# Performance work log

Hardware: AMD Instinct MI355X
Metric: run time of the kernel (lower is better)

The kernel has to match this reference:

```python
import jax, jax.numpy as jnp
import numpy as np

N_P, N_W = 50000, 10000          # protein / pathway node counts
D_P, D_W = 256, 128              # input feature dims
HID, OUT, K, L = 64, 8, 4, 2     # hidden, out, heads, layers
E_PP, E_PW, E_WP = 500000, 150000, 150000


def setup_inputs() -> dict:
    ks = jax.random.split(jax.random.key(0), 16)
    s = 0.1

    def edges(k, e, n_src, n_dst):
        k1, k2 = jax.random.split(k)
        return jnp.stack([
            jax.random.randint(k1, (e,), 0, n_src, dtype=jnp.int32),
            jax.random.randint(k2, (e,), 0, n_dst, dtype=jnp.int32),
        ])

    return {
        "x_protein": jax.random.normal(ks[0], (N_P, D_P), jnp.float32),
        "x_pathway": jax.random.normal(ks[1], (N_W, D_W), jnp.float32),
        "W_proj_p": jax.random.normal(ks[2], (D_P, HID), jnp.float32) * s,
        "b_proj_p": jnp.zeros((HID,), jnp.float32),
        "W_proj_w": jax.random.normal(ks[3], (D_W, HID), jnp.float32) * s,
        "b_proj_w": jnp.zeros((HID,), jnp.float32),
        # per layer, per edge type (0: p->p, 1: p->w, 2: w->p)
        "W_src": jax.random.normal(ks[4], (L, 3, HID, K * HID), jnp.float32) * s,
        "W_dst": jax.random.normal(ks[5], (L, 3, HID, K * HID), jnp.float32) * s,
        "att_src": jax.random.normal(ks[6], (L, 3, K, HID), jnp.float32) * s,
        "att_dst": jax.random.normal(ks[7], (L, 3, K, HID), jnp.float32) * s,
        "conv_bias": jnp.zeros((L, 3, HID), jnp.float32),
        "W_post_p": jax.random.normal(ks[8], (HID, OUT), jnp.float32) * s,
        "b_post_p": jnp.zeros((OUT,), jnp.float32),
        "W_post_w": jax.random.normal(ks[9], (HID, OUT), jnp.float32) * s,
        "b_post_w": jnp.zeros((OUT,), jnp.float32),
        "ei_pp": edges(ks[10], E_PP, N_P, N_P),
        "ei_pw": edges(ks[11], E_PW, N_P, N_W),
        "ei_wp": edges(ks[12], E_WP, N_W, N_P),
    }


def _gat(h_src, h_dst, edge, Wsrc, Wdst, asrc, adst, bias, n_dst):
    """PyG GATConv((-1,-1), HID, heads=K, concat=False, add_self_loops=False)."""
    hs = (h_src @ Wsrc).reshape(-1, K, HID)           # [Ns, K, H]
    hd = (h_dst @ Wdst).reshape(-1, K, HID)           # [Nd, K, H]
    a_s = jnp.sum(hs * asrc, axis=-1)                 # [Ns, K]
    a_d = jnp.sum(hd * adst, axis=-1)                 # [Nd, K]
    src, dst = edge[0], edge[1]
    e = jax.nn.leaky_relu(a_s[src] + a_d[dst], 0.2)   # [E, K]
    # segment softmax over destination neighborhoods
    m = jax.ops.segment_max(e, dst, num_segments=n_dst)
    ex = jnp.exp(e - m[dst])
    denom = jax.ops.segment_sum(ex, dst, num_segments=n_dst)
    alpha = ex / denom[dst]                           # [E, K]
    msg = hs[src] * alpha[:, :, None]                 # [E, K, H]
    out = jax.ops.segment_sum(msg, dst, num_segments=n_dst)  # [Nd, K, H]
    return out.mean(axis=1) + bias                    # concat=False -> head mean


def reference(x_protein, x_pathway, W_proj_p, b_proj_p, W_proj_w, b_proj_w,
              W_src, W_dst, att_src, att_dst, conv_bias,
              W_post_p, b_post_p, W_post_w, b_post_w,
              ei_pp, ei_pw, ei_wp):
    # eval mode: all dropouts are identity
    h_p = x_protein @ W_proj_p + b_proj_p
    h_w = x_pathway @ W_proj_w + b_proj_w
    for l in range(L):
        o_pp = _gat(h_p, h_p, ei_pp, W_src[l, 0], W_dst[l, 0],
                    att_src[l, 0], att_dst[l, 0], conv_bias[l, 0], N_P)
        o_pw = _gat(h_p, h_w, ei_pw, W_src[l, 1], W_dst[l, 1],
                    att_src[l, 1], att_dst[l, 1], conv_bias[l, 1], N_W)
        o_wp = _gat(h_w, h_p, ei_wp, W_src[l, 2], W_dst[l, 2],
                    att_src[l, 2], att_dst[l, 2], conv_bias[l, 2], N_P)
        # HeteroConv aggr='mean': protein receives p->p and w->p; pathway receives p->w
        h_p = jax.nn.elu((o_pp + o_wp) * 0.5)
        h_w = jax.nn.elu(o_pw)
    out_p = h_p @ W_post_p + b_post_p
    out_w = h_w @ W_post_w + b_post_w
    return out_p, out_w
```

## Files before the change

kernel.cpp:

```cpp
#include <hip/hip_runtime.h>
#include <hip/hip_fp16.h>
#include <cfloat>
#include <cmath>

#define N_P 50000
#define N_W 10000
#define D_P 256
#define D_W 128
#define HID 64
#define OUTD 8
#define KH 4
#define LL 2
#define E_PP 500000
#define E_PW 150000
#define E_WP 150000
#define NTOT (N_P + N_W + N_P)
#define ETOT (E_PP + E_PW + E_WP)
#define NBP ((N_P + 63) / 64)
#define NBW ((N_W + 63) / 64)

typedef _Float16 f16x8 __attribute__((ext_vector_type(8)));
typedef float f32x4 __attribute__((ext_vector_type(4)));

__device__ inline float lrelu02(float v) { return v > 0.f ? v : 0.2f * v; }

__device__ inline f16x8 ld8h(const _Float16* p) { return *(const f16x8*)p; }
__device__ inline f16x8 ld8h(const __half* p) { return *(const f16x8*)p; }
__device__ inline f16x8 ld8h(const float* p) {
    float4 lo = *(const float4*)p;
    float4 hi = *(const float4*)(p + 4);
    f16x8 a = { (_Float16)lo.x, (_Float16)lo.y, (_Float16)lo.z, (_Float16)lo.w,
                (_Float16)hi.x, (_Float16)hi.y, (_Float16)hi.z, (_Float16)hi.w };
    return a;
}

template<typename AT, bool ELU>
__device__ inline void gemm64_core(const AT* __restrict__ A, const __half* __restrict__ Bt,
                                   const float* __restrict__ bias,
                                   float* __restrict__ C, __half* __restrict__ C16,
                                   int M, int K, int bid) {
    int lane = threadIdx.x & 63;
    int wv = threadIdx.x >> 6;
    int rbase = bid * 64 + wv * 16;
    int arow = min(rbase + (lane & 15), M - 1);
    int kgrp = (lane >> 4) * 8;
    const AT* Ap = A + (size_t)arow * K + kgrp;
    const _Float16* Bp = (const _Float16*)Bt + kgrp;
    int bcol = lane & 15;

    f32x4 acc0 = {0.f, 0.f, 0.f, 0.f};
    f32x4 acc1 = {0.f, 0.f, 0.f, 0.f};
    f32x4 acc2 = {0.f, 0.f, 0.f, 0.f};
    f32x4 acc3 = {0.f, 0.f, 0.f, 0.f};

#pragma unroll 4
    for (int k0 = 0; k0 < K; k0 += 32) {
        f16x8 a = ld8h(Ap + k0);
        f16x8 b0 = *(const f16x8*)(Bp + (size_t)(0 * 16 + bcol) * K + k0);
        f16x8 b1 = *(const f16x8*)(Bp + (size_t)(1 * 16 + bcol) * K + k0);
        f16x8 b2 = *(const f16x8*)(Bp + (size_t)(2 * 16 + bcol) * K + k0);
        f16x8 b3 = *(const f16x8*)(Bp + (size_t)(3 * 16 + bcol) * K + k0);
        acc0 = __builtin_amdgcn_mfma_f32_16x16x32_f16(a, b0, acc0, 0, 0, 0);
        acc1 = __builtin_amdgcn_mfma_f32_16x16x32_f16(a, b1, acc1, 0, 0, 0);
        acc2 = __builtin_amdgcn_mfma_f32_16x16x32_f16(a, b2, acc2, 0, 0, 0);
        acc3 = __builtin_amdgcn_mfma_f32_16x16x32_f16(a, b3, acc3, 0, 0, 0);
    }

    int crow = rbase + (lane >> 4) * 4;
    f32x4 accs[4] = {acc0, acc1, acc2, acc3};
#pragma unroll
    for (int t = 0; t < 4; ++t) {
        int col = t * 16 + (lane & 15);
        float bv = bias[col];
#pragma unroll
        for (int r = 0; r < 4; ++r) {
            int rr = crow + r;
            if (rr < M) {
                float v = accs[t][r] + bv;
                if (ELU) v = v > 0.f ? v : expf(v) - 1.f;
                C[(size_t)rr * 64 + col] = v;
                C16[(size_t)rr * 64 + col] = __float2half(v);
            }
        }
    }
}

__global__ __launch_bounds__(256) void mfma_proj2(
    const float* __restrict__ xp, const float* __restrict__ xw,
    const __half* __restrict__ wtP, const __half* __restrict__ wtW,
    const float* __restrict__ bpp, const float* __restrict__ bpw,
    float* __restrict__ hp, __half* __restrict__ hp16,
    float* __restrict__ hw, __half* __restrict__ hw16) {
    if (blockIdx.x < NBP)
        gemm64_core<float, false>(xp, wtP, bpp, hp, hp16, N_P, D_P, blockIdx.x);
    else
        gemm64_core<float, false>(xw, wtW, bpw, hw, hw16, N_W, D_W, blockIdx.x - NBP);
}

__global__ __launch_bounds__(256) void mfma_postagg2(
    const __half* __restrict__ aggp, const __half* __restrict__ aggw,
    const __half* __restrict__ wtp, const __half* __restrict__ wtw,
    const float* __restrict__ bp, const float* __restrict__ bw,
    float* __restrict__ hp, __half* __restrict__ hp16,
    float* __restrict__ hw, __half* __restrict__ hw16) {
    if (blockIdx.x < NBP)
        gemm64_core<__half, true>(aggp, wtp, bp, hp, hp16, N_P, 512, blockIdx.x);
    else
        gemm64_core<__half, true>(aggw, wtw, bw, hw, hw16, N_W, 256, blockIdx.x - NBP);
}

__device__ inline void agg_range(int base, int len, const int* __restrict__ perm,
                                 const float4* __restrict__ alpha,
                                 const __half* __restrict__ h16,
                                 int lane, int wv,
                                 float4 (*s_al)[64], int (*s_sr)[64],
                                 float& a0, float& a1, float& a2, float& a3) {
    for (int c0 = 0; c0 < len; c0 += 64) {
        int i = c0 + lane;
        if (i < len) {
            s_sr[wv][lane] = perm[base + i];
            s_al[wv][lane] = alpha[base + i];
        }
        int cnt = min(64, len - c0);
        int j = 0;
        for (; j + 4 <= cnt; j += 4) {
            int sj0 = s_sr[wv][j], sj1 = s_sr[wv][j + 1];
            int sj2 = s_sr[wv][j + 2], sj3 = s_sr[wv][j + 3];
            float h0 = __half2float(h16[(size_t)sj0 * HID + lane]);
            float h1 = __half2float(h16[(size_t)sj1 * HID + lane]);
            float h2 = __half2float(h16[(size_t)sj2 * HID + lane]);
            float h3 = __half2float(h16[(size_t)sj3 * HID + lane]);
            float4 l0 = s_al[wv][j], l1 = s_al[wv][j + 1];
            float4 l2 = s_al[wv][j + 2], l3 = s_al[wv][j + 3];
            a0 = fmaf(l0.x, h0, a0); a1 = fmaf(l0.y, h0, a1);
            a2 = fmaf(l0.z, h0, a2); a3 = fmaf(l0.w, h0, a3);
            a0 = fmaf(l1.x, h1, a0); a1 = fmaf(l1.y, h1, a1);
            a2 = fmaf(l1.z, h1, a2); a3 = fmaf(l1.w, h1, a3);
            a0 = fmaf(l2.x, h2, a0); a1 = fmaf(l2.y, h2, a1);
            a2 = fmaf(l2.z, h2, a2); a3 = fmaf(l2.w, h2, a3);
            a0 = fmaf(l3.x, h3, a0); a1 = fmaf(l3.y, h3, a1);
            a2 = fmaf(l3.z, h3, a2); a3 = fmaf(l3.w, h3, a3);
        }
        for (; j < cnt; ++j) {
            int sj = s_sr[wv][j];
            float4 al = s_al[wv][j];
            float hv = __half2float(h16[(size_t)sj * HID + lane]);
            a0 = fmaf(al.x, hv, a0); a1 = fmaf(al.y, hv, a1);
            a2 = fmaf(al.z, hv, a2); a3 = fmaf(al.w, hv, a3);
        }
    }
}

__global__ __launch_bounds__(256) void gat_msg_all(
    const int* __restrict__ rowptr, const int* __restrict__ perm,
    const float4* __restrict__ alpha, const float4* __restrict__ inv,
    const __half* __restrict__ hp16, const __half* __restrict__ hw16,
    __half* __restrict__ agg_p, __half* __restrict__ agg_w) {
    __shared__ float4 s_al[4][64];
    __shared__ int s_sr[4][64];
    int lane = threadIdx.x & 63;
    int wv = threadIdx.x >> 6;
    int d = (blockIdx.x << 2) + wv;
    if (d >= N_P + N_W) return;

    if (d < N_P) {
        float a0 = 0.f, a1 = 0.f, a2 = 0.f, a3 = 0.f;
        float b0 = 0.f, b1 = 0.f, b2 = 0.f, b3 = 0.f;
        int g1 = d, g2 = N_P + N_W + d;
        int base1 = rowptr[g1], len1 = rowptr[g1 + 1] - base1;
        int base2 = rowptr[g2], len2 = rowptr[g2 + 1] - base2;
        agg_range(base1, len1, perm, alpha, hp16, lane, wv, s_al, s_sr, a0, a1, a2, a3);
        agg_range(base2, len2, perm, alpha, hw16, lane, wv, s_al, s_sr, b0, b1, b2, b3);
        float4 i1 = inv[g1], i2 = inv[g2];
        size_t ob = (size_t)d * 512 + lane;
        agg_p[ob]       = __float2half(a0 * i1.x);
        agg_p[ob + 64]  = __float2half(a1 * i1.y);
        agg_p[ob + 128] = __float2half(a2 * i1.z);
        agg_p[ob + 192] = __float2half(a3 * i1.w);
        agg_p[ob + 256] = __float2half(b0 * i2.x);
        agg_p[ob + 320] = __float2half(b1 * i2.y);
        agg_p[ob + 384] = __float2half(b2 * i2.z);
        agg_p[ob + 448] = __float2half(b3 * i2.w);
    } else {
        int d2 = d - N_P;
        int g = N_P + d2;
        float a0 = 0.f, a1 = 0.f, a2 = 0.f, a3 = 0.f;
        int base = rowptr[g], len = rowptr[g + 1] - base;
        agg_range(base, len, perm, alpha, hp16, lane, wv, s_al, s_sr, a0, a1, a2, a3);
        float4 iv = inv[g];
        size_t ob = (size_t)d2 * 256 + lane;
        agg_w[ob]       = __float2half(a0 * iv.x);
        agg_w[ob + 64]  = __float2half(a1 * iv.y);
        agg_w[ob + 128] = __float2half(a2 * iv.z);
        agg_w[ob + 192] = __float2half(a3 * iv.w);
    }
}

template<int NJ>
__global__ void av_multi(const float* __restrict__ h,
                         const float* __restrict__ W0, const float* __restrict__ W1,
                         const float* __restrict__ W2, const float* __restrict__ W3,
                         float4* __restrict__ o0, float4* __restrict__ o1,
                         float4* __restrict__ o2, float4* __restrict__ o3, int M) {
    int n = blockIdx.x * blockDim.x + threadIdx.x;
    if (n >= M) return;
    const float4* h4 = (const float4*)(h + (size_t)n * HID);
    float a0[4] = {0.f, 0.f, 0.f, 0.f}, a1[4] = {0.f, 0.f, 0.f, 0.f};
    float a2[4] = {0.f, 0.f, 0.f, 0.f}, a3[4] = {0.f, 0.f, 0.f, 0.f};
#pragma unroll
    for (int k4 = 0; k4 < 16; ++k4) {
        float4 hv = h4[k4];
        float hvv[4] = {hv.x, hv.y, hv.z, hv.w};
#pragma unroll
        for (int r = 0; r < 4; ++r) {
            int f = k4 * 4 + r;
            float x = hvv[r];
#pragma unroll
            for (int c = 0; c < 4; ++c) a0[c] = fmaf(x, W0[f * 4 + c], a0[c]);
#pragma unroll
            for (int c = 0; c < 4; ++c) a1[c] = fmaf(x, W1[f * 4 + c], a1[c]);
            if (NJ > 2) {
#pragma unroll
                for (int c = 0; c < 4; ++c) a2[c] = fmaf(x, W2[f * 4 + c], a2[c]);
#pragma unroll
                for (int c = 0; c < 4; ++c) a3[c] = fmaf(x, W3[f * 4 + c], a3[c]);
            }
        }
    }
    o0[n] = make_float4(a0[0], a0[1], a0[2], a0[3]);
    o1[n] = make_float4(a1[0], a1[1], a1[2], a1[3]);
    if (NJ > 2) {
        o2[n] = make_float4(a2[0], a2[1], a2[2], a2[3]);
        o3[n] = make_float4(a3[0], a3[1], a3[2], a3[3]);
    }
}

__global__ void wv_kernel(const float* __restrict__ W, const float* __restrict__ att,
                          float* __restrict__ wv) {
    int lt = blockIdx.x;
    int j = threadIdx.x >> 2, k = threadIdx.x & 3;
    const float* Wp = W + (size_t)lt * HID * (KH * HID) + (size_t)j * (KH * HID) + k * HID;
    const float* ap = att + (size_t)lt * KH * HID + k * HID;
    float s = 0.f;
    for (int h = 0; h < HID; ++h) s += Wp[h] * ap[h];
    wv[(size_t)lt * HID * KH + j * KH + k] = s;
}

__global__ void build_wt_proj(const float* __restrict__ Wpp, const float* __restrict__ Wpw,
                              __half* __restrict__ wtP, __half* __restrict__ wtW) {
    int t = blockIdx.x * blockDim.x + threadIdx.x;
    if (t < 64 * 256) {
        int c = t >> 8, k = t & 255;
        wtP[t] = __float2half(Wpp[k * 64 + c]);
    } else if (t < 64 * 256 + 64 * 128) {
        int u = t - 64 * 256;
        int c = u >> 7, k = u & 127;
        wtW[u] = __float2half(Wpw[k * 64 + c]);
    }
}

__global__ void build_wcomb16(const float* __restrict__ Wsrc, const float* __restrict__ cbias,
                              __half* __restrict__ wtp, float* __restrict__ bp,
                              __half* __restrict__ wtw, float* __restrict__ bw) {
    int t = blockIdx.x * blockDim.x + threadIdx.x;
    const int P = LL * 64 * 512;
    if (t < P) {
        int l = t / (64 * 512);
        int rem = t % (64 * 512);
        int h = rem >> 9, r = rem & 511;
        int part = r >> 8, k = (r & 255) >> 6, j = r & 63;
        int type = (part == 0) ? 0 : 2;
        wtp[t] = __float2half(Wsrc[(((size_t)l * 3 + type) * 64 + j) * 256 + k * 64 + h] * 0.125f);
    } else if (t < P + LL * 64 * 256) {
        int u = t - P;
        int l = u / (64 * 256);
        int rem = u % (64 * 256);
        int h = rem >> 8, r = rem & 255;
        int k = r >> 6, j = r & 63;
        wtw[u] = __float2half(Wsrc[(((size_t)l * 3 + 1) * 64 + j) * 256 + k * 64 + h] * 0.25f);
    }
    if (t < LL * 64) {
        int l = t >> 6, c = t & 63;
        bp[t] = 0.5f * (cbias[(l * 3 + 0) * 64 + c] + cbias[(l * 3 + 2) * 64 + c]);
        bw[t] = cbias[(l * 3 + 1) * 64 + c];
    }
}

__global__ void count3_kernel(const int* __restrict__ ei_pp, const int* __restrict__ ei_pw,
                              const int* __restrict__ ei_wp, int* __restrict__ cnt) {
    int e = blockIdx.x * blockDim.x + threadIdx.x;
    if (e >= ETOT) return;
    const int* ei; int eo, no, E;
    if (e < E_PP) { ei = ei_pp; eo = 0; no = 0; E = E_PP; }
    else if (e < E_PP + E_PW) { ei = ei_pw; eo = E_PP; no = N_P; E = E_PW; }
    else { ei = ei_wp; eo = E_PP + E_PW; no = N_P + N_W; E = E_WP; }
    int el = e - eo;
    atomicAdd(&cnt[no + ei[E + el]], 1);
}

__global__ __launch_bounds__(1024) void block_sum_kernel(const int* __restrict__ cnt,
                                                         int* __restrict__ bsum, int n) {
    __shared__ int wsum[16];
    int tid = threadIdx.x, lane = tid & 63, wv = tid >> 6;
    int i = blockIdx.x * 1024 + tid;
    int v = (i < n) ? cnt[i] : 0;
#pragma unroll
    for (int off = 32; off > 0; off >>= 1) v += __shfl_xor(v, off, 64);
    if (lane == 0) wsum[wv] = v;
    __syncthreads();
    if (tid == 0) {
        int t = 0;
#pragma unroll
        for (int k = 0; k < 16; ++k) t += wsum[k];
        bsum[blockIdx.x] = t;
    }
}

__global__ __launch_bounds__(1024) void scan_bsums_kernel(int* __restrict__ bsum, int nb) {
    __shared__ int wsum[16], wexc[16];
    int tid = threadIdx.x, lane = tid & 63, wv = tid >> 6;
    int v = (tid < nb) ? bsum[tid] : 0;
    int x = v;
#pragma unroll
    for (int off = 1; off < 64; off <<= 1) {
        int y = __shfl_up(x, off, 64);
        if (lane >= off) x += y;
    }
    if (lane == 63) wsum[wv] = x;
    __syncthreads();
    if (wv == 0 && lane < 16) {
        int s = wsum[lane];
        int xx = s;
#pragma unroll
        for (int off = 1; off < 16; off <<= 1) {
            int y = __shfl_up(xx, off, 16);
            if (lane >= off) xx += y;
        }
        wexc[lane] = xx - s;
    }
    __syncthreads();
    if (tid < nb) bsum[tid] = x - v + wexc[wv];
}

__global__ __launch_bounds__(1024) void block_scan_kernel(const int* __restrict__ cnt,
                                                          const int* __restrict__ bsum,
                                                          int* __restrict__ rowptr,
                                                          int* __restrict__ woff, int n) {
    __shared__ int wsum[16], wexc[16];
    int tid = threadIdx.x, lane = tid & 63, wv = tid >> 6;
    int i = blockIdx.x * 1024 + tid;
    int v = (i < n) ? cnt[i] : 0;
    int x = v;
#pragma unroll
    for (int off = 1; off < 64; off <<= 1) {
        int y = __shfl_up(x, off, 64);
        if (lane >= off) x += y;
    }
    if (lane == 63) wsum[wv] = x;
    __syncthreads();
    if (wv == 0 && lane < 16) {
        int s = wsum[lane];
        int xx = s;
#pragma unroll
        for (int off = 1; off < 16; off <<= 1) {
            int y = __shfl_up(xx, off, 16);
            if (lane >= off) xx += y;
        }
        wexc[lane] = xx - s;
    }
    __syncthreads();
    int excl = x - v + wexc[wv] + bsum[blockIdx.x];
    if (i < n) { rowptr[i] = excl; woff[i] = excl; }
    if (i == n - 1) rowptr[n] = excl + v;
}

__global__ void scatter3_kernel(const int* __restrict__ ei_pp, const int* __restrict__ ei_pw,
                                const int* __restrict__ ei_wp, int* __restrict__ woff,
                                int* __restrict__ perm) {
    int e = blockIdx.x * blockDim.x + threadIdx.x;
    if (e >= ETOT) return;
    const int* ei; int eo, no, E;
    if (e < E_PP) { ei = ei_pp; eo = 0; no = 0; E = E_PP; }
    else if (e < E_PP + E_PW) { ei = ei_pw; eo = E_PP; no = N_P; E = E_PW; }
    else { ei = ei_wp; eo = E_PP + E_PW; no = N_P + N_W; E = E_WP; }
    int el = e - eo;
    int p = atomicAdd(&woff[no + ei[E + el]], 1);
    perm[p] = ei[el];
}

__global__ void gat_stats3(const int* __restrict__ rowptr, const int* __restrict__ perm,
                           const float4* __restrict__ a_pp_s, const float4* __restrict__ a_pp_d,
                           const float4* __restrict__ a_pw_s, const float4* __restrict__ a_pw_d,
                           const float4* __restrict__ a_wp_s, const float4* __restrict__ a_wp_d,
                           float4* __restrict__ alpha, float4* __restrict__ inv) {
    int g = blockIdx.x * blockDim.x + threadIdx.x;
    if (g >= NTOT) return;
    const float4 *as, *ad; int d;
    if (g < N_P) { as = a_pp_s; ad = a_pp_d; d = g; }
    else if (g < N_P + N_W) { as = a_pw_s; ad = a_pw_d; d = g - N_P; }
    else { as = a_wp_s; ad = a_wp_d; d = g - (N_P + N_W); }
    int base = rowptr[g], end = rowptr[g + 1];
    float4 adv = ad[d];
    float4 sm = make_float4(0.f, 0.f, 0.f, 0.f);
    for (int i = base; i < end; ++i) {
        float4 asv = as[perm[i]];
        float4 t;
        t.x = __expf(lrelu02(asv.x + adv.x));
        t.y = __expf(lrelu02(asv.y + adv.y));
        t.z = __expf(lrelu02(asv.z + adv.z));
        t.w = __expf(lrelu02(asv.w + adv.w));
        alpha[i] = t;
        sm.x += t.x; sm.y += t.y; sm.z += t.z; sm.w += t.w;
    }
    float4 iv;
    int len = end - base;
    iv.x = len ? 1.f / sm.x : 0.f;
    iv.y = len ? 1.f / sm.y : 0.f;
    iv.z = len ? 1.f / sm.z : 0.f;
    iv.w = len ? 1.f / sm.w : 0.f;
    inv[g] = iv;
}

__global__ void post_out(const float* __restrict__ h_p, const float* __restrict__ h_w,
                         const float* __restrict__ Wp, const float* __restrict__ bpv,
                         const float* __restrict__ Ww, const float* __restrict__ bwv,
                         float* __restrict__ out) {
    int n = blockIdx.x * blockDim.x + threadIdx.x;
    if (n >= N_P + N_W) return;
    const float *h, *W, *bb; float* o;
    if (n < N_P) { h = h_p + (size_t)n * HID; W = Wp; bb = bpv; o = out + (size_t)n * OUTD; }
    else { int m = n - N_P; h = h_w + (size_t)m * HID; W = Ww; bb = bwv; o = out + (size_t)N_P * OUTD + (size_t)m * OUTD; }
    const float4* h4 = (const float4*)h;
    float acc[OUTD];
#pragma unroll
    for (int c = 0; c < OUTD; ++c) acc[c] = bb[c];
#pragma unroll
    for (int k4 = 0; k4 < HID / 4; ++k4) {
        float4 hv = h4[k4];
#pragma unroll
        for (int c = 0; c < OUTD; ++c) {
            acc[c] = fmaf(hv.x, W[(k4 * 4 + 0) * OUTD + c], acc[c]);
            acc[c] = fmaf(hv.y, W[(k4 * 4 + 1) * OUTD + c], acc[c]);
            acc[c] = fmaf(hv.z, W[(k4 * 4 + 2) * OUTD + c], acc[c]);
            acc[c] = fmaf(hv.w, W[(k4 * 4 + 3) * OUTD + c], acc[c]);
        }
    }
#pragma unroll
    for (int c4 = 0; c4 < OUTD / 4; ++c4)
        *(float4*)&o[c4 * 4] = make_float4(acc[c4 * 4], acc[c4 * 4 + 1], acc[c4 * 4 + 2], acc[c4 * 4 + 3]);
}

extern "C" void kernel_launch(void* const* d_in, const int* in_sizes, int n_in,
                              void* d_out, int out_size, void* d_ws, size_t ws_size,
                              hipStream_t stream) {
    const float* x_p    = (const float*)d_in[0];
    const float* x_w    = (const float*)d_in[1];
    const float* Wpp    = (const float*)d_in[2];
    const float* bpp    = (const float*)d_in[3];
    const float* Wpw    = (const float*)d_in[4];
    const float* bpw    = (const float*)d_in[5];
    const float* Wsrc   = (const float*)d_in[6];
    const float* Wdst   = (const float*)d_in[7];
    const float* Asrc   = (const float*)d_in[8];
    const float* Adst   = (const float*)d_in[9];
    const float* cbias  = (const float*)d_in[10];
    const float* Wpostp = (const float*)d_in[11];
    const float* bpostp = (const float*)d_in[12];
    const float* Wpostw = (const float*)d_in[13];
    const float* bpostw = (const float*)d_in[14];
    const int*   ei_pp  = (const int*)d_in[15];
    const int*   ei_pw  = (const int*)d_in[16];
    const int*   ei_wp  = (const int*)d_in[17];

    char* base = (char*)d_ws;
    size_t off = 0;
    auto alloc = [&](size_t bytes) -> void* {
        void* p = base + off;
        off = (off + bytes + 15) & ~(size_t)15;
        return p;
    };

    float*  hp[2];  hp[0]  = (float*)alloc((size_t)N_P * HID * 4);
                    hp[1]  = (float*)alloc((size_t)N_P * HID * 4);
    float*  hw[2];  hw[0]  = (float*)alloc((size_t)N_W * HID * 4);
                    hw[1]  = (float*)alloc((size_t)N_W * HID * 4);
    __half* hp16[2]; hp16[0] = (__half*)alloc((size_t)N_P * HID * 2);
                     hp16[1] = (__half*)alloc((size_t)N_P * HID * 2);
    __half* hw16[2]; hw16[0] = (__half*)alloc((size_t)N_W * HID * 2);
                     hw16[1] = (__half*)alloc((size_t)N_W * HID * 2);
    __half* agg_p  = (__half*)alloc((size_t)N_P * 512 * 2);
    __half* agg_w  = (__half*)alloc((size_t)N_W * 256 * 2);
    float*  wv_s   = (float*)alloc((size_t)LL * 3 * HID * KH * 4);
    float*  wv_d   = (float*)alloc((size_t)LL * 3 * HID * KH * 4);
    __half* wtP    = (__half*)alloc(64 * 256 * 2);
    __half* wtW    = (__half*)alloc(64 * 128 * 2);
    __half* wtp    = (__half*)alloc((size_t)LL * 64 * 512 * 2);
    __half* wtw    = (__half*)alloc((size_t)LL * 64 * 256 * 2);
    float*  bp     = (float*)alloc(LL * 64 * 4);
    float*  bw     = (float*)alloc(LL * 64 * 4);
    float*  a_pp_s = (float*)alloc((size_t)N_P * KH * 4);
    float*  a_pp_d = (float*)alloc((size_t)N_P * KH * 4);
    float*  a_pw_s = (float*)alloc((size_t)N_P * KH * 4);
    float*  a_pw_d = (float*)alloc((size_t)N_W * KH * 4);
    float*  a_wp_s = (float*)alloc((size_t)N_W * KH * 4);
    float*  a_wp_d = (float*)alloc((size_t)N_P * KH * 4);
    float*  alpha  = (float*)alloc((size_t)ETOT * KH * 4);
    float*  inv    = (float*)alloc((size_t)NTOT * KH * 4);
    int*    cnt    = (int*)alloc((size_t)NTOT * 4);
    int*    woff   = (int*)alloc((size_t)NTOT * 4);
    int*    rowptr = (int*)alloc(((size_t)NTOT + 1) * 4);
    int*    perm   = (int*)alloc((size_t)ETOT * 4);
    int*    bsum   = (int*)alloc(1024 * 4);

    auto cdiv = [](long long a, long long b) { return (int)((a + b - 1) / b); };

    wv_kernel<<<LL * 3, 256, 0, stream>>>(Wsrc, Asrc, wv_s);
    wv_kernel<<<LL * 3, 256, 0, stream>>>(Wdst, Adst, wv_d);
    build_wt_proj<<<cdiv(64 * 256 + 64 * 128, 256), 256, 0, stream>>>(Wpp, Wpw, wtP, wtW);
    build_wcomb16<<<cdiv(LL * 64 * (512 + 256), 256), 256, 0, stream>>>(Wsrc, cbias, wtp, bp, wtw, bw);

    int nb = cdiv(NTOT, 1024);
    (void)hipMemsetAsync(cnt, 0, (size_t)NTOT * 4, stream);
    count3_kernel<<<cdiv(ETOT, 256), 256, 0, stream>>>(ei_pp, ei_pw, ei_wp, cnt);
    block_sum_kernel<<<nb, 1024, 0, stream>>>(cnt, bsum, NTOT);
    scan_bsums_kernel<<<1, 1024, 0, stream>>>(bsum, nb);
    block_scan_kernel<<<nb, 1024, 0, stream>>>(cnt, bsum, rowptr, woff, NTOT);
    scatter3_kernel<<<cdiv(ETOT, 256), 256, 0, stream>>>(ei_pp, ei_pw, ei_wp, woff, perm);

    mfma_proj2<<<NBP + NBW, 256, 0, stream>>>(x_p, x_w, wtP, wtW, bpp, bpw,
                                              hp[0], hp16[0], hw[0], hw16[0]);

    int cur = 0;
    for (int l = 0; l < LL; ++l) {
        int lt0 = l * 3 + 0, lt1 = l * 3 + 1, lt2 = l * 3 + 2;
        av_multi<4><<<cdiv(N_P, 256), 256, 0, stream>>>(
            hp[cur], wv_s + (size_t)lt0 * 256, wv_d + (size_t)lt0 * 256,
            wv_s + (size_t)lt1 * 256, wv_d + (size_t)lt2 * 256,
            (float4*)a_pp_s, (float4*)a_pp_d, (float4*)a_pw_s, (float4*)a_wp_d, N_P);
        av_multi<2><<<cdiv(N_W, 256), 256, 0, stream>>>(
            hw[cur], wv_d + (size_t)lt1 * 256, wv_s + (size_t)lt2 * 256, nullptr, nullptr,
            (float4*)a_pw_d, (float4*)a_wp_s, nullptr, nullptr, N_W);

        gat_stats3<<<cdiv(NTOT, 256), 256, 0, stream>>>(
            rowptr, perm,
            (const float4*)a_pp_s, (const float4*)a_pp_d,
            (const float4*)a_pw_s, (const float4*)a_pw_d,
            (const float4*)a_wp_s, (const float4*)a_wp_d,
            (float4*)alpha, (float4*)inv);

        gat_msg_all<<<cdiv(N_P + N_W, 4), 256, 0, stream>>>(
            rowptr, perm, (const float4*)alpha, (const float4*)inv,
            hp16[cur], hw16[cur], agg_p, agg_w);

        mfma_postagg2<<<NBP + NBW, 256, 0, stream>>>(
            agg_p, agg_w, wtp + (size_t)l * 64 * 512, wtw + (size_t)l * 64 * 256,
            bp + l * 64, bw + l * 64,
            hp[cur ^ 1], hp16[cur ^ 1], hw[cur ^ 1], hw16[cur ^ 1]);
        cur ^= 1;
    }

    post_out<<<cdiv(N_P + N_W, 256), 256, 0, stream>>>(
        hp[cur], hw[cur], Wpostp, bpostp, Wpostw, bpostw, (float*)d_out);
}
```

Baseline: 372.9 us.

## Build CSR via two-level bucket sort with shared-memory local sort

Replaces the per-node global atomic count, three-kernel scan and per-node atomic scatter with a coarse 256-node bucket count, a single-block bucket scan, a scatter into bucket-ordered temp pairs, and a per-bucket kernel that builds the local histogram, rowptr and perm using shared-memory atomics. The aim is fewer launches and less contention and scattered traffic on global atomics. In exchange the bucket-level atomics are highly contended, and an extra 8-byte temp array must be written and read back twice. Edge order within each row becomes nondeterministic, as it already was with the atomic scatter.

```diff
diff --git a/kernel.cpp b/kernel.cpp
--- a/kernel.cpp
+++ b/kernel.cpp
@@ -18,6 +18,7 @@
 #define ETOT (E_PP + E_PW + E_WP)
 #define NBP ((N_P + 63) / 64)
 #define NBW ((N_W + 63) / 64)
+#define NBKT ((NTOT + 255) / 256)
 
 typedef _Float16 f16x8 __attribute__((ext_vector_type(8)));
 typedef float f32x4 __attribute__((ext_vector_type(4)));
@@ -286,8 +287,8 @@
     }
 }
 
-__global__ void count3_kernel(const int* __restrict__ ei_pp, const int* __restrict__ ei_pw,
-                              const int* __restrict__ ei_wp, int* __restrict__ cnt) {
+__global__ void count_bucket(const int* __restrict__ ei_pp, const int* __restrict__ ei_pw,
+                             const int* __restrict__ ei_wp, int* __restrict__ bcnt) {
     int e = blockIdx.x * blockDim.x + threadIdx.x;
     if (e >= ETOT) return;
     const int* ei; int eo, no, E;
@@ -295,31 +296,16 @@
     else if (e < E_PP + E_PW) { ei = ei_pw; eo = E_PP; no = N_P; E = E_PW; }
     else { ei = ei_wp; eo = E_PP + E_PW; no = N_P + N_W; E = E_WP; }
     int el = e - eo;
-    atomicAdd(&cnt[no + ei[E + el]], 1);
-}
-
-__global__ __launch_bounds__(1024) void block_sum_kernel(const int* __restrict__ cnt,
-                                                         int* __restrict__ bsum, int n) {
-    __shared__ int wsum[16];
+    int g = no + ei[E + el];
+    atomicAdd(&bcnt[g >> 8], 1);
+}
+
+__global__ __launch_bounds__(512) void scan_buckets(const int* __restrict__ bcnt,
+                                                    int* __restrict__ bbase,
+                                                    int* __restrict__ bwoff) {
+    __shared__ int wsum[8], wexc[8];
     int tid = threadIdx.x, lane = tid & 63, wv = tid >> 6;
-    int i = blockIdx.x * 1024 + tid;
-    int v = (i < n) ? cnt[i] : 0;
-#pragma unroll
-    for (int off = 32; off > 0; off >>= 1) v += __shfl_xor(v, off, 64);
-    if (lane == 0) wsum[wv] = v;
-    __syncthreads();
-    if (tid == 0) {
-        int t = 0;
-#pragma unroll
-        for (int k = 0; k < 16; ++k) t += wsum[k];
-        bsum[blockIdx.x] = t;
-    }
-}
-
-__global__ __launch_bounds__(1024) void scan_bsums_kernel(int* __restrict__ bsum, int nb) {
-    __shared__ int wsum[16], wexc[16];
-    int tid = threadIdx.x, lane = tid & 63, wv = tid >> 6;
-    int v = (tid < nb) ? bsum[tid] : 0;
+    int v = (tid < NBKT) ? bcnt[tid] : 0;
     int x = v;
 #pragma unroll
     for (int off = 1; off < 64; off <<= 1) {
@@ -328,55 +314,25 @@
     }
     if (lane == 63) wsum[wv] = x;
     __syncthreads();
-    if (wv == 0 && lane < 16) {
+    if (wv == 0 && lane < 8) {
         int s = wsum[lane];
         int xx = s;
 #pragma unroll
-        for (int off = 1; off < 16; off <<= 1) {
-            int y = __shfl_up(xx, off, 16);
+        for (int off = 1; off < 8; off <<= 1) {
+            int y = __shfl_up(xx, off, 8);
             if (lane >= off) xx += y;
         }
         wexc[lane] = xx - s;
     }
     __syncthreads();
-    if (tid < nb) bsum[tid] = x - v + wexc[wv];
-}
-
-__global__ __launch_bounds__(1024) void block_scan_kernel(const int* __restrict__ cnt,
-                                                          const int* __restrict__ bsum,
-                                                          int* __restrict__ rowptr,
-                                                          int* __restrict__ woff, int n) {
-    __shared__ int wsum[16], wexc[16];
-    int tid = threadIdx.x, lane = tid & 63, wv = tid >> 6;
-    int i = blockIdx.x * 1024 + tid;
-    int v = (i < n) ? cnt[i] : 0;
-    int x = v;
-#pragma unroll
-    for (int off = 1; off < 64; off <<= 1) {
-        int y = __shfl_up(x, off, 64);
-        if (lane >= off) x += y;
-    }
-    if (lane == 63) wsum[wv] = x;
-    __syncthreads();
-    if (wv == 0 && lane < 16) {
-        int s = wsum[lane];
-        int xx = s;
-#pragma unroll
-        for (int off = 1; off < 16; off <<= 1) {
-            int y = __shfl_up(xx, off, 16);
-            if (lane >= off) xx += y;
-        }
-        wexc[lane] = xx - s;
-    }
-    __syncthreads();
-    int excl = x - v + wexc[wv] + bsum[blockIdx.x];
-    if (i < n) { rowptr[i] = excl; woff[i] = excl; }
-    if (i == n - 1) rowptr[n] = excl + v;
-}
-
-__global__ void scatter3_kernel(const int* __restrict__ ei_pp, const int* __restrict__ ei_pw,
-                                const int* __restrict__ ei_wp, int* __restrict__ woff,
-                                int* __restrict__ perm) {
+    int excl = x - v + wexc[wv];
+    if (tid < NBKT) { bbase[tid] = excl; bwoff[tid] = excl; }
+    if (tid == NBKT - 1) bbase[NBKT] = excl + v;
+}
+
+__global__ void scatter_bucket(const int* __restrict__ ei_pp, const int* __restrict__ ei_pw,
+                               const int* __restrict__ ei_wp, int* __restrict__ bwoff,
+                               int2* __restrict__ temp) {
     int e = blockIdx.x * blockDim.x + threadIdx.x;
     if (e >= ETOT) return;
     const int* ei; int eo, no, E;
@@ -384,8 +340,49 @@
     else if (e < E_PP + E_PW) { ei = ei_pw; eo = E_PP; no = N_P; E = E_PW; }
     else { ei = ei_wp; eo = E_PP + E_PW; no = N_P + N_W; E = E_WP; }
     int el = e - eo;
-    int p = atomicAdd(&woff[no + ei[E + el]], 1);
-    perm[p] = ei[el];
+    int g = no + ei[E + el];
+    int p = atomicAdd(&bwoff[g >> 8], 1);
+    temp[p] = make_int2(g, ei[el]);
+}
+
+__global__ __launch_bounds__(256) void bucket_sort(const int2* __restrict__ temp,
+                                                   const int* __restrict__ bbase,
+                                                   int* __restrict__ rowptr,
+                                                   int* __restrict__ perm) {
+    __shared__ int hist[256];
+    __shared__ int offs[256];
+    __shared__ int wtot[4];
+    int b = blockIdx.x;
+    int tid = threadIdx.x;
+    int bstart = bbase[b], bend = bbase[b + 1];
+    hist[tid] = 0;
+    __syncthreads();
+    for (int i = bstart + tid; i < bend; i += 256)
+        atomicAdd(&hist[temp[i].x & 255], 1);
+    __syncthreads();
+    int v = hist[tid];
+    int lane = tid & 63, wv = tid >> 6;
+    int x = v;
+#pragma unroll
+    for (int off = 1; off < 64; off <<= 1) {
+        int y = __shfl_up(x, off, 64);
+        if (lane >= off) x += y;
+    }
+    if (lane == 63) wtot[wv] = x;
+    __syncthreads();
+    int add = 0;
+#pragma unroll
+    for (int k = 0; k < 4; ++k) add += (k < wv) ? wtot[k] : 0;
+    int excl = x - v + add;
+    int d_global = b * 256 + tid;
+    if (d_global <= NTOT) rowptr[d_global] = bstart + excl;
+    offs[tid] = excl;
+    __syncthreads();
+    for (int i = bstart + tid; i < bend; i += 256) {
+        int2 t = temp[i];
+        int r = atomicAdd(&offs[t.x & 255], 1);
+        perm[bstart + r] = t.y;
+    }
 }
 
 __global__ void gat_stats3(const int* __restrict__ rowptr, const int* __restrict__ perm,
@@ -506,11 +503,12 @@
     float*  a_wp_d = (float*)alloc((size_t)N_P * KH * 4);
     float*  alpha  = (float*)alloc((size_t)ETOT * KH * 4);
     float*  inv    = (float*)alloc((size_t)NTOT * KH * 4);
-    int*    cnt    = (int*)alloc((size_t)NTOT * 4);
-    int*    woff   = (int*)alloc((size_t)NTOT * 4);
     int*    rowptr = (int*)alloc(((size_t)NTOT + 1) * 4);
     int*    perm   = (int*)alloc((size_t)ETOT * 4);
-    int*    bsum   = (int*)alloc(1024 * 4);
+    int*    bcnt   = (int*)alloc((NBKT + 1) * 4);
+    int*    bbase  = (int*)alloc((NBKT + 1) * 4);
+    int*    bwoff  = (int*)alloc((NBKT + 1) * 4);
+    int2*   temp   = (int2*)alloc((size_t)ETOT * 8);
 
     auto cdiv = [](long long a, long long b) { return (int)((a + b - 1) / b); };
 
@@ -519,13 +517,11 @@
     build_wt_proj<<<cdiv(64 * 256 + 64 * 128, 256), 256, 0, stream>>>(Wpp, Wpw, wtP, wtW);
     build_wcomb16<<<cdiv(LL * 64 * (512 + 256), 256), 256, 0, stream>>>(Wsrc, cbias, wtp, bp, wtw, bw);
 
-    int nb = cdiv(NTOT, 1024);
-    (void)hipMemsetAsync(cnt, 0, (size_t)NTOT * 4, stream);
-    count3_kernel<<<cdiv(ETOT, 256), 256, 0, stream>>>(ei_pp, ei_pw, ei_wp, cnt);
-    block_sum_kernel<<<nb, 1024, 0, stream>>>(cnt, bsum, NTOT);
-    scan_bsums_kernel<<<1, 1024, 0, stream>>>(bsum, nb);
-    block_scan_kernel<<<nb, 1024, 0, stream>>>(cnt, bsum, rowptr, woff, NTOT);
-    scatter3_kernel<<<cdiv(ETOT, 256), 256, 0, stream>>>(ei_pp, ei_pw, ei_wp, woff, perm);
+    (void)hipMemsetAsync(bcnt, 0, (NBKT + 1) * 4, stream);
+    count_bucket<<<cdiv(ETOT, 256), 256, 0, stream>>>(ei_pp, ei_pw, ei_wp, bcnt);
+    scan_buckets<<<1, 512, 0, stream>>>(bcnt, bbase, bwoff);
+    scatter_bucket<<<cdiv(ETOT, 256), 256, 0, stream>>>(ei_pp, ei_pw, ei_wp, bwoff, temp);
+    bucket_sort<<<NBKT, 256, 0, stream>>>(temp, bbase, rowptr, perm);
 
     mfma_proj2<<<NBP + NBW, 256, 0, stream>>>(x_p, x_w, wtP, wtW, bpp, bpw,
                                               hp[0], hp16[0], hw[0], hw16[0]);
```

Result: slower. 1.161 ms (+211.3%).

## Fuse GAT softmax stats into message aggregation kernel

Applied to the files above, without the earlier changes.

Removes the separate per-destination stats kernel that wrote exp-attention coefficients and inverse sums to global memory. The aggregation wave now computes leaky-relu/exp coefficients on the fly per edge chunk, accumulates per-head sums with a wave reduction, and normalizes at the end. This drops a kernel launch and the alpha/inv global round trip, and replaces a serial per-thread edge loop with wave-parallel work. The cost is a gather of the source attention scores inside the aggregation kernel.

```diff
diff --git a/kernel.cpp b/kernel.cpp
--- a/kernel.cpp
+++ b/kernel.cpp
@@ -109,17 +109,26 @@
         gemm64_core<__half, true>(aggw, wtw, bw, hw, hw16, N_W, 256, blockIdx.x - NBP);
 }
 
-__device__ inline void agg_range(int base, int len, const int* __restrict__ perm,
-                                 const float4* __restrict__ alpha,
-                                 const __half* __restrict__ h16,
-                                 int lane, int wv,
-                                 float4 (*s_al)[64], int (*s_sr)[64],
-                                 float& a0, float& a1, float& a2, float& a3) {
+__device__ inline void agg_range_f(int base, int len, const int* __restrict__ perm,
+                                   const float4* __restrict__ as4, float4 adv,
+                                   const __half* __restrict__ h16,
+                                   int lane, int wv,
+                                   float4 (*s_al)[64], int (*s_sr)[64],
+                                   float& a0, float& a1, float& a2, float& a3,
+                                   float4& sm) {
     for (int c0 = 0; c0 < len; c0 += 64) {
         int i = c0 + lane;
         if (i < len) {
-            s_sr[wv][lane] = perm[base + i];
-            s_al[wv][lane] = alpha[base + i];
+            int s = perm[base + i];
+            float4 asv = as4[s];
+            float4 t;
+            t.x = __expf(lrelu02(asv.x + adv.x));
+            t.y = __expf(lrelu02(asv.y + adv.y));
+            t.z = __expf(lrelu02(asv.z + adv.z));
+            t.w = __expf(lrelu02(asv.w + adv.w));
+            s_sr[wv][lane] = s;
+            s_al[wv][lane] = t;
+            sm.x += t.x; sm.y += t.y; sm.z += t.z; sm.w += t.w;
         }
         int cnt = min(64, len - c0);
         int j = 0;
@@ -151,9 +160,22 @@
     }
 }
 
-__global__ __launch_bounds__(256) void gat_msg_all(
+__device__ inline float4 wave_sum4(float4 v) {
+#pragma unroll
+    for (int off = 32; off > 0; off >>= 1) {
+        v.x += __shfl_xor(v.x, off, 64);
+        v.y += __shfl_xor(v.y, off, 64);
+        v.z += __shfl_xor(v.z, off, 64);
+        v.w += __shfl_xor(v.w, off, 64);
+    }
+    return v;
+}
+
+__global__ __launch_bounds__(256) void gat_msg_fused(
     const int* __restrict__ rowptr, const int* __restrict__ perm,
-    const float4* __restrict__ alpha, const float4* __restrict__ inv,
+    const float4* __restrict__ a_pp_s, const float4* __restrict__ a_pp_d,
+    const float4* __restrict__ a_pw_s, const float4* __restrict__ a_pw_d,
+    const float4* __restrict__ a_wp_s, const float4* __restrict__ a_wp_d,
     const __half* __restrict__ hp16, const __half* __restrict__ hw16,
     __half* __restrict__ agg_p, __half* __restrict__ agg_w) {
     __shared__ float4 s_al[4][64];
@@ -166,12 +188,26 @@
     if (d < N_P) {
         float a0 = 0.f, a1 = 0.f, a2 = 0.f, a3 = 0.f;
         float b0 = 0.f, b1 = 0.f, b2 = 0.f, b3 = 0.f;
+        float4 sm1 = make_float4(0.f, 0.f, 0.f, 0.f);
+        float4 sm2 = make_float4(0.f, 0.f, 0.f, 0.f);
         int g1 = d, g2 = N_P + N_W + d;
         int base1 = rowptr[g1], len1 = rowptr[g1 + 1] - base1;
         int base2 = rowptr[g2], len2 = rowptr[g2 + 1] - base2;
-        agg_range(base1, len1, perm, alpha, hp16, lane, wv, s_al, s_sr, a0, a1, a2, a3);
-        agg_range(base2, len2, perm, alpha, hw16, lane, wv, s_al, s_sr, b0, b1, b2, b3);
-        float4 i1 = inv[g1], i2 = inv[g2];
+        agg_range_f(base1, len1, perm, a_pp_s, a_pp_d[d], hp16, lane, wv,
+                    s_al, s_sr, a0, a1, a2, a3, sm1);
+        agg_range_f(base2, len2, perm, a_wp_s, a_wp_d[d], hw16, lane, wv,
+                    s_al, s_sr, b0, b1, b2, b3, sm2);
+        sm1 = wave_sum4(sm1);
+        sm2 = wave_sum4(sm2);
+        float4 i1, i2;
+        i1.x = len1 ? 1.f / sm1.x : 0.f;
+        i1.y = len1 ? 1.f / sm1.y : 0.f;
+        i1.z = len1 ? 1.f / sm1.z : 0.f;
+        i1.w = len1 ? 1.f / sm1.w : 0.f;
+        i2.x = len2 ? 1.f / sm2.x : 0.f;
+        i2.y = len2 ? 1.f / sm2.y : 0.f;
+        i2.z = len2 ? 1.f / sm2.z : 0.f;
+        i2.w = len2 ? 1.f / sm2.w : 0.f;
         size_t ob = (size_t)d * 512 + lane;
         agg_p[ob]       = __float2half(a0 * i1.x);
         agg_p[ob + 64]  = __float2half(a1 * i1.y);
@@ -185,9 +221,16 @@
         int d2 = d - N_P;
         int g = N_P + d2;
         float a0 = 0.f, a1 = 0.f, a2 = 0.f, a3 = 0.f;
+        float4 sm = make_float4(0.f, 0.f, 0.f, 0.f);
         int base = rowptr[g], len = rowptr[g + 1] - base;
-        agg_range(base, len, perm, alpha, hp16, lane, wv, s_al, s_sr, a0, a1, a2, a3);
-        float4 iv = inv[g];
+        agg_range_f(base, len, perm, a_pw_s, a_pw_d[d2], hp16, lane, wv,
+                    s_al, s_sr, a0, a1, a2, a3, sm);
+        sm = wave_sum4(sm);
+        float4 iv;
+        iv.x = len ? 1.f / sm.x : 0.f;
+        iv.y = len ? 1.f / sm.y : 0.f;
+        iv.z = len ? 1.f / sm.z : 0.f;
+        iv.w = len ? 1.f / sm.w : 0.f;
         size_t ob = (size_t)d2 * 256 + lane;
         agg_w[ob]       = __float2half(a0 * iv.x);
         agg_w[ob + 64]  = __float2half(a1 * iv.y);
@@ -386,39 +429,6 @@
     int el = e - eo;
     int p = atomicAdd(&woff[no + ei[E + el]], 1);
     perm[p] = ei[el];
-}
-
-__global__ void gat_stats3(const int* __restrict__ rowptr, const int* __restrict__ perm,
-                           const float4* __restrict__ a_pp_s, const float4* __restrict__ a_pp_d,
-                           const float4* __restrict__ a_pw_s, const float4* __restrict__ a_pw_d,
-                           const float4* __restrict__ a_wp_s, const float4* __restrict__ a_wp_d,
-                           float4* __restrict__ alpha, float4* __restrict__ inv) {
-    int g = blockIdx.x * blockDim.x + threadIdx.x;
-    if (g >= NTOT) return;
-    const float4 *as, *ad; int d;
-    if (g < N_P) { as = a_pp_s; ad = a_pp_d; d = g; }
-    else if (g < N_P + N_W) { as = a_pw_s; ad = a_pw_d; d = g - N_P; }
-    else { as = a_wp_s; ad = a_wp_d; d = g - (N_P + N_W); }
-    int base = rowptr[g], end = rowptr[g + 1];
-    float4 adv = ad[d];
-    float4 sm = make_float4(0.f, 0.f, 0.f, 0.f);
-    for (int i = base; i < end; ++i) {
-        float4 asv = as[perm[i]];
-        float4 t;
-        t.x = __expf(lrelu02(asv.x + adv.x));
-        t.y = __expf(lrelu02(asv.y + adv.y));
-        t.z = __expf(lrelu02(asv.z + adv.z));
-        t.w = __expf(lrelu02(asv.w + adv.w));
-        alpha[i] = t;
-        sm.x += t.x; sm.y += t.y; sm.z += t.z; sm.w += t.w;
-    }
-    float4 iv;
-    int len = end - base;
-    iv.x = len ? 1.f / sm.x : 0.f;
-    iv.y = len ? 1.f / sm.y : 0.f;
-    iv.z = len ? 1.f / sm.z : 0.f;
-    iv.w = len ? 1.f / sm.w : 0.f;
-    inv[g] = iv;
 }
 
 __global__ void post_out(const float* __restrict__ h_p, const float* __restrict__ h_w,
@@ -504,8 +514,6 @@
     float*  a_pw_d = (float*)alloc((size_t)N_W * KH * 4);
     float*  a_wp_s = (float*)alloc((size_t)N_W * KH * 4);
     float*  a_wp_d = (float*)alloc((size_t)N_P * KH * 4);
-    float*  alpha  = (float*)alloc((size_t)ETOT * KH * 4);
-    float*  inv    = (float*)alloc((size_t)NTOT * KH * 4);
     int*    cnt    = (int*)alloc((size_t)NTOT * 4);
     int*    woff   = (int*)alloc((size_t)NTOT * 4);
     int*    rowptr = (int*)alloc(((size_t)NTOT + 1) * 4);
@@ -541,15 +549,11 @@
             hw[cur], wv_d + (size_t)lt1 * 256, wv_s + (size_t)lt2 * 256, nullptr, nullptr,
             (float4*)a_pw_d, (float4*)a_wp_s, nullptr, nullptr, N_W);
 
-        gat_stats3<<<cdiv(NTOT, 256), 256, 0, stream>>>(
+        gat_msg_fused<<<cdiv(N_P + N_W, 4), 256, 0, stream>>>(
             rowptr, perm,
             (const float4*)a_pp_s, (const float4*)a_pp_d,
             (const float4*)a_pw_s, (const float4*)a_pw_d,
             (const float4*)a_wp_s, (const float4*)a_wp_d,
-            (float4*)alpha, (float4*)inv);
-
-        gat_msg_all<<<cdiv(N_P + N_W, 4), 256, 0, stream>>>(
-            rowptr, perm, (const float4*)alpha, (const float4*)inv,
             hp16[cur], hw16[cur], agg_p, agg_w);
 
         mfma_postagg2<<<NBP + NBW, 256, 0, stream>>>(
```

Result: faster. 360.0 us (-3.5%).
